# Kernel optimization log

Hardware: AMD Instinct MI355X
Metric: run time of the kernel (lower is better)

The kernel has to match this reference:

```python
import jax, jax.numpy as jnp
import numpy as np

TEMP = 10.0  # softmax_ called with N=10.0 in reduce_func

def qmul(a, b):
    # Hamilton product, rows are (w, x, y, z)
    aw, ax, ay, az = a[..., 0], a[..., 1], a[..., 2], a[..., 3]
    bw, bx, by, bz = b[..., 0], b[..., 1], b[..., 2], b[..., 3]
    return jnp.stack([
        aw * bw - ax * bx - ay * by - az * bz,
        aw * bx + ax * bw + ay * bz - az * by,
        aw * by - ax * bz + ay * bw + az * bx,
        aw * bz + ax * by - ay * bx + az * bw,
    ], axis=-1)

def setup_inputs() -> dict:
    key = jax.random.key(0)
    k1, k2, k3, k4, k5, k6 = jax.random.split(key, 6)
    N, E = 100000, 3200000
    node_levels = jax.random.uniform(k1, (N,), dtype=jnp.float32)
    node_q = jax.random.normal(k2, (N, 4), dtype=jnp.float32)
    node_q = node_q / jnp.linalg.norm(node_q, axis=1, keepdims=True)
    edge_rel_q = jax.random.normal(k3, (E, 4), dtype=jnp.float32)
    edge_rel_q = edge_rel_q / jnp.linalg.norm(edge_rel_q, axis=1, keepdims=True)
    edge_w = jax.random.uniform(k4, (E,), dtype=jnp.float32)
    src = jax.random.randint(k5, (E,), 0, N, dtype=jnp.int32)
    dst = jax.random.randint(k6, (E,), 0, N, dtype=jnp.int32)
    return {"node_levels": node_levels, "node_q": node_q,
            "edge_rel_q": edge_rel_q, "edge_w": edge_w,
            "src": src, "dst": dst}

def reference(node_levels, node_q, edge_rel_q, edge_w, src, dst):
    N = node_q.shape[0]
    # per-edge message: accumulated quaternion rel_q * q_src
    accu_q = qmul(edge_rel_q, node_q[src])          # [E,4]
    l_src = node_levels[src]                        # [E]
    # softmax logits: cost = w * l (self term has w = 1)
    cost_e = TEMP * edge_w * l_src                  # [E]
    cost_self = TEMP * node_levels                  # [N]
    # segmented stable softmax over {self} U in-edges per dst node
    seg_max = jax.ops.segment_max(cost_e, dst, num_segments=N)
    m = jnp.maximum(seg_max, cost_self)             # [N]
    exp_e = jnp.exp(cost_e - m[dst])                # [E]
    exp_self = jnp.exp(cost_self - m)               # [N]
    Z = jax.ops.segment_sum(exp_e, dst, num_segments=N) + exp_self
    # weighted sums
    sum_q = jax.ops.segment_sum(exp_e[:, None] * accu_q, dst, num_segments=N) \
            + exp_self[:, None] * node_q            # [N,4]
    sum_l = jax.ops.segment_sum(exp_e * l_src, dst, num_segments=N) \
            + exp_self * node_levels                # [N]
    out_q = sum_q / Z[:, None]
    out_levels = sum_l / Z
    # F.normalize(q, p=2, dim=1) with eps=1e-12 clamp
    norm = jnp.maximum(jnp.linalg.norm(out_q, axis=1, keepdims=True), 1e-12)
    return out_q / norm, out_levels
```

## Files before the change

### kernel.cpp

```cpp
#include <hip/hip_runtime.h>
#include <hip/hip_fp16.h>

#define TEMP 10.0f
#define TPB 512
#define HTPB 256
#define NBLK 768
#define SHIFT 9
#define GSZ 512
#define BMAX 256
#define TILE 2048
#define GTPB 1024
#define CAP 44

typedef float v2f  __attribute__((ext_vector_type(2)));
typedef float vf4  __attribute__((ext_vector_type(4)));
typedef unsigned uv4 __attribute__((ext_vector_type(4)));

__device__ __forceinline__ int   nt_i (const int* p)   { return __builtin_nontemporal_load(p); }
__device__ __forceinline__ float nt_f (const float* p) { return __builtin_nontemporal_load(p); }
__device__ __forceinline__ float4 nt_f4(const float4* p) {
    vf4 v = __builtin_nontemporal_load((const vf4*)p);
    return make_float4(v.x, v.y, v.z, v.w);
}
__device__ __forceinline__ uint4 nt_u4(const uint4* p) {
    uv4 v = __builtin_nontemporal_load((const uv4*)p);
    uint4 r; r.x = v.x; r.y = v.y; r.z = v.z; r.w = v.w; return r;
}

__device__ __forceinline__ void pk_fadd(float* p, float a, float b) {
#if __has_builtin(__builtin_amdgcn_global_atomic_fadd_v2f32)
    v2f v; v.x = a; v.y = b;
    __builtin_amdgcn_global_atomic_fadd_v2f32(
        (__attribute__((address_space(1))) v2f*)p, v);
#else
    atomicAdd(p, a); atomicAdd(p + 1, b);
#endif
}

__device__ __forceinline__ void hamilton(float4 a, float4 b,
                                         float& ow, float& ox, float& oy, float& oz) {
    ow = a.x*b.x - a.y*b.y - a.z*b.z - a.w*b.w;
    ox = a.x*b.y + a.y*b.x + a.z*b.w - a.w*b.z;
    oy = a.x*b.z - a.y*b.w + a.z*b.x + a.w*b.y;
    oz = a.x*b.w + a.y*b.z - a.z*b.y + a.w*b.x;
}

__device__ __forceinline__ unsigned f2h(float x) {
    return (unsigned)__half_as_ushort(__float2half_rn(x));
}
__device__ __forceinline__ float h2f(unsigned u) {
    return __half2float(__ushort_as_half((unsigned short)(u & 0xFFFFu)));
}

__global__ void __launch_bounds__(HTPB)
hist_kernel(const int* __restrict__ dst, unsigned* __restrict__ blkhist,
            int E, int B, int span) {
    extern __shared__ unsigned h[];
    for (int i = threadIdx.x; i < B; i += blockDim.x) h[i] = 0;
    __syncthreads();
    int start = blockIdx.x * span;
    int end = start + span; if (end > E) end = E;
    for (int e = start + threadIdx.x; e < end; e += blockDim.x)
        atomicAdd(&h[((unsigned)nt_i(&dst[e])) >> SHIFT], 1u);
    __syncthreads();
    for (int i = threadIdx.x; i < B; i += blockDim.x)
        blkhist[(size_t)i * gridDim.x + blockIdx.x] = h[i];
}

__global__ void __launch_bounds__(1024)
scan_blocks_kernel(unsigned* __restrict__ blkhist, unsigned* __restrict__ totals) {
    __shared__ unsigned s[1024];
    int b = blockIdx.x, t = threadIdx.x, n = blockDim.x;
    unsigned v = blkhist[(size_t)b * n + t];
    s[t] = v; __syncthreads();
    for (int off = 1; off < n; off <<= 1) {
        unsigned add = (t >= off) ? s[t - off] : 0u;
        __syncthreads();
        s[t] += add;
        __syncthreads();
    }
    blkhist[(size_t)b * n + t] = s[t] - v;
    if (t == n - 1) totals[b] = s[t];
}

__global__ void __launch_bounds__(1024)
scan_totals_kernel(const unsigned* __restrict__ totals,
                   unsigned* __restrict__ offsets, int B) {
    __shared__ unsigned s[1024];
    int t = threadIdx.x;
    unsigned v = (t < B) ? totals[t] : 0u;
    s[t] = v; __syncthreads();
    for (int off = 1; off < 1024; off <<= 1) {
        unsigned add = (t >= off) ? s[t - off] : 0u;
        __syncthreads();
        s[t] += add;
        __syncthreads();
    }
    if (t < B) offsets[t] = s[t] - v;
    if (t == B - 1) offsets[B] = s[t];
}

__global__ void __launch_bounds__(TPB)
scatter_sort_kernel(const float* __restrict__ nl, const float4* __restrict__ nq,
                    const float4* __restrict__ erq, const float* __restrict__ ew,
                    const int* __restrict__ src, const int* __restrict__ dst,
                    const unsigned* __restrict__ blkhist,
                    const unsigned* __restrict__ offsets,
                    uint4* __restrict__ buckets,
                    int E, int B, int span) {
    __shared__ uint4    stage[TILE];
    __shared__ unsigned gslot[TILE];
    __shared__ unsigned gcur[BMAX];
    __shared__ unsigned th[BMAX];
    __shared__ unsigned basec[BMAX];
    __shared__ unsigned curt[BMAX];

    int blk = blockIdx.x, nb = gridDim.x, tid = threadIdx.x;
    for (int b = tid; b < B; b += TPB)
        gcur[b] = offsets[b] + blkhist[(size_t)b * nb + blk];
    int start = blk * span;
    int end = start + span; if (end > E) end = E;

    for (int ts = start; ts < end; ts += TILE) {
        int tE = end - ts; if (tE > TILE) tE = TILE;
        for (int b = tid; b < B; b += TPB) th[b] = 0;
        __syncthreads();
        for (int k = tid; k < tE; k += TPB)
            atomicAdd(&th[((unsigned)dst[ts + k]) >> SHIFT], 1u);
        __syncthreads();
        if (tid < 64) {
            int lane = tid;
            unsigned vals[4];
            unsigned tot = 0;
            #pragma unroll
            for (int c = 0; c < 4; ++c) {
                int i = lane * 4 + c;
                vals[c] = (i < B) ? th[i] : 0u;
                tot += vals[c];
            }
            unsigned inc = tot;
            #pragma unroll
            for (int off = 1; off < 64; off <<= 1) {
                unsigned up = __shfl_up(inc, off);
                if (lane >= off) inc += up;
            }
            unsigned run = inc - tot;
            #pragma unroll
            for (int c = 0; c < 4; ++c) {
                int i = lane * 4 + c;
                if (i < B) { basec[i] = run; curt[i] = run; }
                run += vals[c];
            }
        }
        __syncthreads();
        for (int k = tid; k < tE; k += TPB) {
            int e = ts + k;
            int s_ = nt_i(&src[e]);
            unsigned d = (unsigned)dst[e];
            float l = nl[s_];
            float p = __expf(TEMP * nt_f(&ew[e]) * l);
            float ow, ox, oy, oz;
            hamilton(nt_f4(&erq[e]), nq[s_], ow, ox, oy, oz);
            unsigned b = d >> SHIFT;
            unsigned pos = atomicAdd(&curt[b], 1u);
            uint4 pk;
            pk.x = (d & (GSZ - 1)) | (f2h(p) << 16);
            pk.y = f2h(p * l)  | (f2h(p * ow) << 16);
            pk.z = f2h(p * ox) | (f2h(p * oy) << 16);
            pk.w = f2h(p * oz);
            stage[pos] = pk;
            gslot[pos] = gcur[b] + (pos - basec[b]);
        }
        __syncthreads();
        for (int k = tid; k < tE; k += TPB)
            buckets[gslot[k]] = stage[k];
        __syncthreads();
        for (int b = tid; b < B; b += TPB) gcur[b] += th[b];
        __syncthreads();
    }
}

__global__ void __launch_bounds__(GTPB)
gather_pay_kernel(const float* __restrict__ nl, const float4* __restrict__ nq,
                  const unsigned* __restrict__ offsets,
                  const uint4* __restrict__ buckets,
                  float4* __restrict__ out_q, float* __restrict__ out_l, int N) {
    __shared__ unsigned short idx[GSZ * CAP];
    __shared__ int   curn[GSZ];
    __shared__ float ovf[GSZ * 7];
    int b = blockIdx.x, tid = threadIdx.x;
    for (int i = tid; i < GSZ; i += GTPB) curn[i] = 0;
    for (int i = tid; i < GSZ * 7; i += GTPB) ovf[i] = 0.f;
    __syncthreads();

    unsigned s0 = offsets[b], s1 = offsets[b + 1];
    int M = (int)(s1 - s0);
    const unsigned* bx = (const unsigned*)(buckets + s0);

    for (int i = tid; i < M; i += GTPB) {
        unsigned w0 = bx[4 * (size_t)i];
        unsigned dl = w0 & (GSZ - 1);
        int slot = atomicAdd(&curn[dl], 1);
        if (slot < CAP) {
            idx[dl * CAP + slot] = (unsigned short)i;
        } else {
            uint4 pk = buckets[s0 + i];
            float* a = &ovf[dl * 7];
            atomicAdd(a + 0, h2f(pk.x >> 16));
            atomicAdd(a + 1, h2f(pk.y));
            atomicAdd(a + 2, h2f(pk.y >> 16));
            atomicAdd(a + 3, h2f(pk.z));
            atomicAdd(a + 4, h2f(pk.z >> 16));
            atomicAdd(a + 5, h2f(pk.w));
        }
    }
    __syncthreads();

    for (int half = 0; half < (GSZ * 4) / GTPB; ++half) {
        int j = half * (GTPB / 4) + (tid >> 2);
        int r = tid & 3;
        int deg = curn[j]; if (deg > CAP) deg = CAP;
        float aZ = 0.f, aL = 0.f, a0 = 0.f, a1 = 0.f, a2 = 0.f, a3 = 0.f;
        for (int s = r; s < deg; s += 4) {
            int i = idx[j * CAP + s];
            uint4 pk = nt_u4(&buckets[s0 + i]);
            aZ += h2f(pk.x >> 16);
            aL += h2f(pk.y);
            a0 += h2f(pk.y >> 16);
            a1 += h2f(pk.z);
            a2 += h2f(pk.z >> 16);
            a3 += h2f(pk.w);
        }
        for (int m = 1; m <= 2; m <<= 1) {
            aZ += __shfl_xor(aZ, m); aL += __shfl_xor(aL, m);
            a0 += __shfl_xor(a0, m); a1 += __shfl_xor(a1, m);
            a2 += __shfl_xor(a2, m); a3 += __shfl_xor(a3, m);
        }
        if (r == 0) {
            int n = b * GSZ + j;
            if (n < N) {
                const float* o = &ovf[j * 7];
                float l = nl[n];
                float ps = __expf(TEMP * l);
                float Z  = aZ + o[0] + ps;
                float sl = aL + o[1] + ps * l;
                float4 q = nq[n];
                float qw = a0 + o[2] + ps * q.x;
                float qx = a1 + o[3] + ps * q.y;
                float qy = a2 + o[4] + ps * q.z;
                float qz = a3 + o[5] + ps * q.w;
                float inv = 1.0f / Z;
                qw *= inv; qx *= inv; qy *= inv; qz *= inv;
                float norm = fmaxf(sqrtf(qw*qw + qx*qx + qy*qy + qz*qz), 1e-12f);
                float rn = 1.0f / norm;
                out_q[n] = make_float4(qw * rn, qx * rn, qy * rn, qz * rn);
                out_l[n] = sl * inv;
            }
        }
    }
}

__global__ void __launch_bounds__(256)
scatter_kernel(const int* __restrict__ dst, int* __restrict__ cnt,
               int* __restrict__ bucket, int cap,
               const float* __restrict__ node_levels, const float4* __restrict__ node_q,
               const float4* __restrict__ edge_rel_q, const float* __restrict__ edge_w,
               const int* __restrict__ src, float* __restrict__ side, int E) {
    int e = blockIdx.x * blockDim.x + threadIdx.x;
    if (e >= E) return;
    int d = dst[e];
    int slot = atomicAdd(&cnt[d], 1);
    if (slot < cap) {
        bucket[(long long)d * cap + slot] = e;
    } else {
        int s = src[e];
        float l = node_levels[s];
        float p = __expf(TEMP * edge_w[e] * l);
        float ow, ox, oy, oz;
        hamilton(edge_rel_q[e], node_q[s], ow, ox, oy, oz);
        float* rec = side + 6 * (long long)d;
        pk_fadd(rec + 0, p,      p * l);
        pk_fadd(rec + 2, p * ow, p * ox);
        pk_fadd(rec + 4, p * oy, p * oz);
    }
}

__global__ void __launch_bounds__(256)
gather_kernel(const float* __restrict__ node_levels, const float4* __restrict__ node_q,
              const float4* __restrict__ edge_rel_q, const float* __restrict__ edge_w,
              const int* __restrict__ src, const int* __restrict__ cnt,
              const int* __restrict__ bucket, int cap, const float* __restrict__ side,
              float4* __restrict__ out_q, float* __restrict__ out_l, int N) {
    int tid  = blockIdx.x * blockDim.x + threadIdx.x;
    int wave = tid >> 6, lane = tid & 63, half = lane >> 5, sub = lane & 31;
    int n = wave * 2 + half;
    float aZ = 0.f, aL = 0.f, a0 = 0.f, a1 = 0.f, a2 = 0.f, a3 = 0.f;
    if (n < N) {
        int deg = cnt[n]; if (deg > cap) deg = cap;
        const int* bkt = bucket + (long long)n * cap;
        for (int s = sub; s < deg; s += 32) {
            int e = bkt[s];
            int sn = src[e];
            float l = node_levels[sn];
            float p = __expf(TEMP * edge_w[e] * l);
            float ow, ox, oy, oz;
            hamilton(edge_rel_q[e], node_q[sn], ow, ox, oy, oz);
            aZ += p; aL += p * l; a0 += p * ow; a1 += p * ox; a2 += p * oy; a3 += p * oz;
        }
    }
    for (int m = 16; m; m >>= 1) {
        aZ += __shfl_xor(aZ, m); aL += __shfl_xor(aL, m);
        a0 += __shfl_xor(a0, m); a1 += __shfl_xor(a1, m);
        a2 += __shfl_xor(a2, m); a3 += __shfl_xor(a3, m);
    }
    if (sub == 0 && n < N) {
        const float* rec = side + 6 * (long long)n;
        float l  = node_levels[n];
        float ps = __expf(TEMP * l);
        float Z  = aZ + rec[0] + ps;
        float sl = aL + rec[1] + ps * l;
        float4 q = node_q[n];
        float qw = a0 + rec[2] + ps * q.x;
        float qx = a1 + rec[3] + ps * q.y;
        float qy = a2 + rec[4] + ps * q.z;
        float qz = a3 + rec[5] + ps * q.w;
        float inv = 1.0f / Z;
        qw *= inv; qx *= inv; qy *= inv; qz *= inv;
        float norm = fmaxf(sqrtf(qw*qw + qx*qx + qy*qy + qz*qz), 1e-12f);
        float rn = 1.0f / norm;
        out_q[n] = make_float4(qw * rn, qx * rn, qy * rn, qz * rn);
        out_l[n] = sl * inv;
    }
}

extern "C" void kernel_launch(void* const* d_in, const int* in_sizes, int n_in,
                              void* d_out, int out_size, void* d_ws, size_t ws_size,
                              hipStream_t stream) {
    const float*  node_levels = (const float*)d_in[0];
    const float4* node_q      = (const float4*)d_in[1];
    const float4* edge_rel_q  = (const float4*)d_in[2];
    const float*  edge_w      = (const float*)d_in[3];
    const int*    src         = (const int*)d_in[4];
    const int*    dst         = (const int*)d_in[5];

    const int N = in_sizes[0];
    const int E = in_sizes[3];

    const int B = (N + GSZ - 1) / GSZ;
    const int span = (E + NBLK - 1) / NBLK;

    size_t head_elems   = (size_t)B * NBLK + B + (B + 1);
    size_t buckets_byte = (head_elems * 4 + 15) & ~(size_t)15;
    size_t need         = buckets_byte + (size_t)E * 16;

    bool seg_ok = ((size_t)E / (size_t)B) < 32768;

    if (need <= ws_size && B <= BMAX && seg_ok) {
        unsigned* blkhist = (unsigned*)d_ws;
        unsigned* totals  = blkhist + (size_t)B * NBLK;
        unsigned* offsets = totals + B;
        uint4*    buckets = (uint4*)((char*)d_ws + buckets_byte);

        hist_kernel<<<NBLK, HTPB, B * 4, stream>>>(dst, blkhist, E, B, span);
        scan_blocks_kernel<<<B, NBLK, 0, stream>>>(blkhist, totals);
        scan_totals_kernel<<<1, 1024, 0, stream>>>(totals, offsets, B);
        scatter_sort_kernel<<<NBLK, TPB, 0, stream>>>(
            node_levels, node_q, edge_rel_q, edge_w, src, dst,
            blkhist, offsets, buckets, E, B, span);
        gather_pay_kernel<<<B, GTPB, 0, stream>>>(
            node_levels, node_q, offsets, buckets,
            (float4*)d_out, (float*)d_out + 4 * (long long)N, N);
    } else {
        const int tpb = 256;
        size_t cnt_elems  = ((size_t)N + 3) & ~(size_t)3;
        size_t side_elems = 6 * (size_t)N;
        size_t head_bytes = (cnt_elems + side_elems) * 4;
        int cap = 0;
        for (int c : {128, 64}) {
            if (head_bytes + (size_t)N * c * 4 <= ws_size) { cap = c; break; }
        }
        int*   cnt    = (int*)d_ws;
        float* side   = (float*)d_ws + cnt_elems;
        int*   bucket = (int*)d_ws + cnt_elems + side_elems;
        hipMemsetAsync(d_ws, 0, head_bytes, stream);
        scatter_kernel<<<(E + tpb - 1) / tpb, tpb, 0, stream>>>(
            dst, cnt, bucket, cap, node_levels, node_q, edge_rel_q, edge_w, src, side, E);
        int waves  = (N + 1) / 2;
        int blocks = (waves * 64 + tpb - 1) / tpb;
        gather_kernel<<<blocks, tpb, 0, stream>>>(
            node_levels, node_q, edge_rel_q, edge_w, src, cnt, bucket, cap, side,
            (float4*)d_out, (float*)d_out + 4 * (long long)N, N);
    }
}
```

Measured before the change: 236.7 us.

## Replace histogram-scan bucket sort with atomic slot reservation into fixed-capacity buckets

Drops the separate histogram and two scan kernels. The scatter kernel now reserves per-bucket ranges with global atomics into fixed-capacity buckets, and anything past capacity spills to an overflow FIFO. Buckets shrink to 200 nodes, giving 500 gather blocks, and the payload moves to a 12-byte struct-of-arrays plus a 2-byte local-dst array instead of 16-byte packed records. This removes three launches and a pass over dst in exchange for global atomic contention and a capacity heuristic. Every gather block also scans the whole overflow FIFO, and entries beyond its 8192 limit are silently dropped.

```diff
diff --git a/kernel.cpp b/kernel.cpp
--- a/kernel.cpp
+++ b/kernel.cpp
@@ -1,30 +1,24 @@
 #include <hip/hip_runtime.h>
 #include <hip/hip_fp16.h>
+#include <cmath>
 
 #define TEMP 10.0f
 #define TPB 512
-#define HTPB 256
-#define NBLK 768
-#define SHIFT 9
-#define GSZ 512
-#define BMAX 256
 #define TILE 2048
+#define GSZ 200
+#define BMAX 512
 #define GTPB 1024
 #define CAP 44
+#define OV 8192
 
 typedef float v2f  __attribute__((ext_vector_type(2)));
 typedef float vf4  __attribute__((ext_vector_type(4)));
-typedef unsigned uv4 __attribute__((ext_vector_type(4)));
 
 __device__ __forceinline__ int   nt_i (const int* p)   { return __builtin_nontemporal_load(p); }
 __device__ __forceinline__ float nt_f (const float* p) { return __builtin_nontemporal_load(p); }
 __device__ __forceinline__ float4 nt_f4(const float4* p) {
     vf4 v = __builtin_nontemporal_load((const vf4*)p);
     return make_float4(v.x, v.y, v.z, v.w);
-}
-__device__ __forceinline__ uint4 nt_u4(const uint4* p) {
-    uv4 v = __builtin_nontemporal_load((const uv4*)p);
-    uint4 r; r.x = v.x; r.y = v.y; r.z = v.z; r.w = v.w; return r;
 }
 
 __device__ __forceinline__ void pk_fadd(float* p, float a, float b) {
@@ -52,184 +46,143 @@
     return __half2float(__ushort_as_half((unsigned short)(u & 0xFFFFu)));
 }
 
-__global__ void __launch_bounds__(HTPB)
-hist_kernel(const int* __restrict__ dst, unsigned* __restrict__ blkhist,
-            int E, int B, int span) {
-    extern __shared__ unsigned h[];
-    for (int i = threadIdx.x; i < B; i += blockDim.x) h[i] = 0;
-    __syncthreads();
-    int start = blockIdx.x * span;
-    int end = start + span; if (end > E) end = E;
-    for (int e = start + threadIdx.x; e < end; e += blockDim.x)
-        atomicAdd(&h[((unsigned)nt_i(&dst[e])) >> SHIFT], 1u);
-    __syncthreads();
-    for (int i = threadIdx.x; i < B; i += blockDim.x)
-        blkhist[(size_t)i * gridDim.x + blockIdx.x] = h[i];
-}
-
-__global__ void __launch_bounds__(1024)
-scan_blocks_kernel(unsigned* __restrict__ blkhist, unsigned* __restrict__ totals) {
-    __shared__ unsigned s[1024];
-    int b = blockIdx.x, t = threadIdx.x, n = blockDim.x;
-    unsigned v = blkhist[(size_t)b * n + t];
-    s[t] = v; __syncthreads();
-    for (int off = 1; off < n; off <<= 1) {
-        unsigned add = (t >= off) ? s[t - off] : 0u;
-        __syncthreads();
-        s[t] += add;
-        __syncthreads();
-    }
-    blkhist[(size_t)b * n + t] = s[t] - v;
-    if (t == n - 1) totals[b] = s[t];
-}
-
-__global__ void __launch_bounds__(1024)
-scan_totals_kernel(const unsigned* __restrict__ totals,
-                   unsigned* __restrict__ offsets, int B) {
-    __shared__ unsigned s[1024];
-    int t = threadIdx.x;
-    unsigned v = (t < B) ? totals[t] : 0u;
-    s[t] = v; __syncthreads();
-    for (int off = 1; off < 1024; off <<= 1) {
-        unsigned add = (t >= off) ? s[t - off] : 0u;
-        __syncthreads();
-        s[t] += add;
-        __syncthreads();
-    }
-    if (t < B) offsets[t] = s[t] - v;
-    if (t == B - 1) offsets[B] = s[t];
-}
-
 __global__ void __launch_bounds__(TPB)
-scatter_sort_kernel(const float* __restrict__ nl, const float4* __restrict__ nq,
-                    const float4* __restrict__ erq, const float* __restrict__ ew,
-                    const int* __restrict__ src, const int* __restrict__ dst,
-                    const unsigned* __restrict__ blkhist,
-                    const unsigned* __restrict__ offsets,
-                    uint4* __restrict__ buckets,
-                    int E, int B, int span) {
-    __shared__ uint4    stage[TILE];
-    __shared__ unsigned gslot[TILE];
-    __shared__ unsigned gcur[BMAX];
-    __shared__ unsigned th[BMAX];
-    __shared__ unsigned basec[BMAX];
-    __shared__ unsigned curt[BMAX];
-
-    int blk = blockIdx.x, nb = gridDim.x, tid = threadIdx.x;
-    for (int b = tid; b < B; b += TPB)
-        gcur[b] = offsets[b] + blkhist[(size_t)b * nb + blk];
-    int start = blk * span;
-    int end = start + span; if (end > E) end = E;
-
-    for (int ts = start; ts < end; ts += TILE) {
-        int tE = end - ts; if (tE > TILE) tE = TILE;
-        for (int b = tid; b < B; b += TPB) th[b] = 0;
-        __syncthreads();
-        for (int k = tid; k < tE; k += TPB)
-            atomicAdd(&th[((unsigned)dst[ts + k]) >> SHIFT], 1u);
-        __syncthreads();
-        if (tid < 64) {
-            int lane = tid;
-            unsigned vals[4];
-            unsigned tot = 0;
-            #pragma unroll
-            for (int c = 0; c < 4; ++c) {
-                int i = lane * 4 + c;
-                vals[c] = (i < B) ? th[i] : 0u;
-                tot += vals[c];
+scatter_res_kernel(const float* __restrict__ nl, const float4* __restrict__ nq,
+                   const float4* __restrict__ erq, const float* __restrict__ ew,
+                   const int* __restrict__ src, const int* __restrict__ dst,
+                   unsigned* __restrict__ cnt, unsigned* __restrict__ ovfcur,
+                   uint4* __restrict__ fifo,
+                   unsigned* __restrict__ pay, unsigned short* __restrict__ dlarr,
+                   int E, int B, int capB) {
+    __shared__ unsigned sy[TILE], sz[TILE], sw[TILE], gsl[TILE];
+    __shared__ unsigned short sdl[TILE];
+    __shared__ unsigned th[BMAX], basec[BMAX], curt[BMAX], resv[BMAX];
+
+    int tid = threadIdx.x;
+    int ts = blockIdx.x * TILE;
+    int tE = E - ts; if (tE > TILE) tE = TILE;
+
+    for (int b = tid; b < B; b += TPB) th[b] = 0;
+    __syncthreads();
+    for (int k = tid; k < tE; k += TPB)
+        atomicAdd(&th[((unsigned)dst[ts + k]) / GSZ], 1u);
+    __syncthreads();
+    if (tid < 64) {
+        unsigned vals[8]; unsigned tot = 0;
+        #pragma unroll
+        for (int c = 0; c < 8; ++c) {
+            int i = tid * 8 + c;
+            vals[c] = (i < B) ? th[i] : 0u;
+            tot += vals[c];
+        }
+        unsigned inc = tot;
+        #pragma unroll
+        for (int off = 1; off < 64; off <<= 1) {
+            unsigned up = __shfl_up(inc, off);
+            if (tid >= off) inc += up;
+        }
+        unsigned run = inc - tot;
+        #pragma unroll
+        for (int c = 0; c < 8; ++c) {
+            int i = tid * 8 + c;
+            if (i < B) {
+                basec[i] = run; curt[i] = run;
+                resv[i] = vals[c] ? atomicAdd(&cnt[i], vals[c]) : 0u;
             }
-            unsigned inc = tot;
-            #pragma unroll
-            for (int off = 1; off < 64; off <<= 1) {
-                unsigned up = __shfl_up(inc, off);
-                if (lane >= off) inc += up;
-            }
-            unsigned run = inc - tot;
-            #pragma unroll
-            for (int c = 0; c < 4; ++c) {
-                int i = lane * 4 + c;
-                if (i < B) { basec[i] = run; curt[i] = run; }
-                run += vals[c];
-            }
-        }
-        __syncthreads();
-        for (int k = tid; k < tE; k += TPB) {
-            int e = ts + k;
-            int s_ = nt_i(&src[e]);
-            unsigned d = (unsigned)dst[e];
-            float l = nl[s_];
-            float p = __expf(TEMP * nt_f(&ew[e]) * l);
-            float ow, ox, oy, oz;
-            hamilton(nt_f4(&erq[e]), nq[s_], ow, ox, oy, oz);
-            unsigned b = d >> SHIFT;
-            unsigned pos = atomicAdd(&curt[b], 1u);
-            uint4 pk;
-            pk.x = (d & (GSZ - 1)) | (f2h(p) << 16);
-            pk.y = f2h(p * l)  | (f2h(p * ow) << 16);
-            pk.z = f2h(p * ox) | (f2h(p * oy) << 16);
-            pk.w = f2h(p * oz);
-            stage[pos] = pk;
-            gslot[pos] = gcur[b] + (pos - basec[b]);
-        }
-        __syncthreads();
-        for (int k = tid; k < tE; k += TPB)
-            buckets[gslot[k]] = stage[k];
-        __syncthreads();
-        for (int b = tid; b < B; b += TPB) gcur[b] += th[b];
-        __syncthreads();
+            run += vals[c];
+        }
+    }
+    __syncthreads();
+    for (int k = tid; k < tE; k += TPB) {
+        int e = ts + k;
+        int s_ = nt_i(&src[e]);
+        unsigned d = (unsigned)dst[e];
+        float l = nl[s_];
+        float p = __expf(TEMP * nt_f(&ew[e]) * l);
+        float ow, ox, oy, oz;
+        hamilton(nt_f4(&erq[e]), nq[s_], ow, ox, oy, oz);
+        unsigned bu = d / GSZ;
+        unsigned pos = atomicAdd(&curt[bu], 1u);
+        unsigned y = f2h(p)      | (f2h(p * l)  << 16);
+        unsigned z = f2h(p * ow) | (f2h(p * ox) << 16);
+        unsigned w = f2h(p * oy) | (f2h(p * oz) << 16);
+        sy[pos] = y; sz[pos] = z; sw[pos] = w;
+        sdl[pos] = (unsigned short)(d - bu * GSZ);
+        unsigned off = resv[bu] + (pos - basec[bu]);
+        if (off < (unsigned)capB) {
+            gsl[pos] = bu * (unsigned)capB + off;
+        } else {
+            gsl[pos] = 0xFFFFFFFFu;
+            unsigned o = atomicAdd(ovfcur, 1u);
+            if (o < OV) { uint4 f; f.x = d; f.y = y; f.z = z; f.w = w; fifo[o] = f; }
+        }
+    }
+    __syncthreads();
+    for (int k = tid; k < tE; k += TPB) {
+        unsigned g = gsl[k];
+        if (g != 0xFFFFFFFFu) {
+            size_t base = 3 * (size_t)g;
+            pay[base] = sy[k]; pay[base + 1] = sz[k]; pay[base + 2] = sw[k];
+            dlarr[g] = sdl[k];
+        }
     }
 }
 
 __global__ void __launch_bounds__(GTPB)
-gather_pay_kernel(const float* __restrict__ nl, const float4* __restrict__ nq,
-                  const unsigned* __restrict__ offsets,
-                  const uint4* __restrict__ buckets,
+gather_seg_kernel(const float* __restrict__ nl, const float4* __restrict__ nq,
+                  const unsigned* __restrict__ cnt, const unsigned* __restrict__ ovfcur,
+                  const uint4* __restrict__ fifo,
+                  const unsigned* __restrict__ pay, const unsigned short* __restrict__ dlarr,
+                  int capB,
                   float4* __restrict__ out_q, float* __restrict__ out_l, int N) {
     __shared__ unsigned short idx[GSZ * CAP];
     __shared__ int   curn[GSZ];
-    __shared__ float ovf[GSZ * 7];
+    __shared__ float ovfa[GSZ * 7];
     int b = blockIdx.x, tid = threadIdx.x;
     for (int i = tid; i < GSZ; i += GTPB) curn[i] = 0;
-    for (int i = tid; i < GSZ * 7; i += GTPB) ovf[i] = 0.f;
-    __syncthreads();
-
-    unsigned s0 = offsets[b], s1 = offsets[b + 1];
-    int M = (int)(s1 - s0);
-    const unsigned* bx = (const unsigned*)(buckets + s0);
+    for (int i = tid; i < GSZ * 7; i += GTPB) ovfa[i] = 0.f;
+    __syncthreads();
+
+    int M = (int)cnt[b]; if (M > capB) M = capB;
+    const unsigned* pb = pay + 3 * (size_t)b * capB;
+    const unsigned short* db = dlarr + (size_t)b * capB;
 
     for (int i = tid; i < M; i += GTPB) {
-        unsigned w0 = bx[4 * (size_t)i];
-        unsigned dl = w0 & (GSZ - 1);
+        int dl = db[i];
         int slot = atomicAdd(&curn[dl], 1);
         if (slot < CAP) {
             idx[dl * CAP + slot] = (unsigned short)i;
         } else {
-            uint4 pk = buckets[s0 + i];
-            float* a = &ovf[dl * 7];
-            atomicAdd(a + 0, h2f(pk.x >> 16));
-            atomicAdd(a + 1, h2f(pk.y));
-            atomicAdd(a + 2, h2f(pk.y >> 16));
-            atomicAdd(a + 3, h2f(pk.z));
-            atomicAdd(a + 4, h2f(pk.z >> 16));
-            atomicAdd(a + 5, h2f(pk.w));
-        }
-    }
-    __syncthreads();
-
-    for (int half = 0; half < (GSZ * 4) / GTPB; ++half) {
-        int j = half * (GTPB / 4) + (tid >> 2);
-        int r = tid & 3;
+            unsigned y = pb[3*(size_t)i], z = pb[3*(size_t)i+1], w = pb[3*(size_t)i+2];
+            float* a = &ovfa[dl * 7];
+            atomicAdd(a + 0, h2f(y)); atomicAdd(a + 1, h2f(y >> 16));
+            atomicAdd(a + 2, h2f(z)); atomicAdd(a + 3, h2f(z >> 16));
+            atomicAdd(a + 4, h2f(w)); atomicAdd(a + 5, h2f(w >> 16));
+        }
+    }
+    unsigned on = *ovfcur; if (on > OV) on = OV;
+    for (unsigned i = tid; i < on; i += GTPB) {
+        uint4 f = fifo[i];
+        unsigned loc = f.x - (unsigned)b * GSZ;
+        if (loc < GSZ) {
+            float* a = &ovfa[loc * 7];
+            atomicAdd(a + 0, h2f(f.y)); atomicAdd(a + 1, h2f(f.y >> 16));
+            atomicAdd(a + 2, h2f(f.z)); atomicAdd(a + 3, h2f(f.z >> 16));
+            atomicAdd(a + 4, h2f(f.w)); atomicAdd(a + 5, h2f(f.w >> 16));
+        }
+    }
+    __syncthreads();
+
+    int j = tid >> 2, r = tid & 3;
+    if (j < GSZ) {
         int deg = curn[j]; if (deg > CAP) deg = CAP;
         float aZ = 0.f, aL = 0.f, a0 = 0.f, a1 = 0.f, a2 = 0.f, a3 = 0.f;
         for (int s = r; s < deg; s += 4) {
             int i = idx[j * CAP + s];
-            uint4 pk = nt_u4(&buckets[s0 + i]);
-            aZ += h2f(pk.x >> 16);
-            aL += h2f(pk.y);
-            a0 += h2f(pk.y >> 16);
-            a1 += h2f(pk.z);
-            a2 += h2f(pk.z >> 16);
-            a3 += h2f(pk.w);
+            unsigned y = pb[3*(size_t)i], z = pb[3*(size_t)i+1], w = pb[3*(size_t)i+2];
+            aZ += h2f(y); aL += h2f(y >> 16);
+            a0 += h2f(z); a1 += h2f(z >> 16);
+            a2 += h2f(w); a3 += h2f(w >> 16);
         }
         for (int m = 1; m <= 2; m <<= 1) {
             aZ += __shfl_xor(aZ, m); aL += __shfl_xor(aL, m);
@@ -239,7 +192,7 @@
         if (r == 0) {
             int n = b * GSZ + j;
             if (n < N) {
-                const float* o = &ovf[j * 7];
+                const float* o = &ovfa[j * 7];
                 float l = nl[n];
                 float ps = __expf(TEMP * l);
                 float Z  = aZ + o[0] + ps;
@@ -347,28 +300,30 @@
     const int E = in_sizes[3];
 
     const int B = (N + GSZ - 1) / GSZ;
-    const int span = (E + NBLK - 1) / NBLK;
-
-    size_t head_elems   = (size_t)B * NBLK + B + (B + 1);
-    size_t buckets_byte = (head_elems * 4 + 15) & ~(size_t)15;
-    size_t need         = buckets_byte + (size_t)E * 16;
-
-    bool seg_ok = ((size_t)E / (size_t)B) < 32768;
-
-    if (need <= ws_size && B <= BMAX && seg_ok) {
-        unsigned* blkhist = (unsigned*)d_ws;
-        unsigned* totals  = blkhist + (size_t)B * NBLK;
-        unsigned* offsets = totals + B;
-        uint4*    buckets = (uint4*)((char*)d_ws + buckets_byte);
-
-        hist_kernel<<<NBLK, HTPB, B * 4, stream>>>(dst, blkhist, E, B, span);
-        scan_blocks_kernel<<<B, NBLK, 0, stream>>>(blkhist, totals);
-        scan_totals_kernel<<<1, 1024, 0, stream>>>(totals, offsets, B);
-        scatter_sort_kernel<<<NBLK, TPB, 0, stream>>>(
+
+    size_t fifo_off = (((size_t)(B + 1) * 4) + 15) & ~(size_t)15;
+    size_t pay_off  = fifo_off + (size_t)OV * 16;
+
+    long long availCap = ((long long)ws_size - (long long)pay_off) / (14LL * B);
+    int meanB  = E / B;
+    int minCap = meanB + 6 * (int)std::sqrt((double)meanB) + 8;
+    int capB   = (availCap > 16000) ? 16000 : (int)availCap;
+
+    if (capB >= minCap && B <= BMAX && meanB < 32000) {
+        unsigned*       cnt    = (unsigned*)d_ws;
+        unsigned*       ovfc   = cnt + B;
+        uint4*          fifo   = (uint4*)((char*)d_ws + fifo_off);
+        unsigned*       pay    = (unsigned*)((char*)d_ws + pay_off);
+        unsigned short* dlarr  = (unsigned short*)((char*)d_ws + pay_off + 12ull * B * capB);
+
+        hipMemsetAsync(d_ws, 0, (size_t)(B + 1) * 4, stream);
+
+        int nblk = (E + TILE - 1) / TILE;
+        scatter_res_kernel<<<nblk, TPB, 0, stream>>>(
             node_levels, node_q, edge_rel_q, edge_w, src, dst,
-            blkhist, offsets, buckets, E, B, span);
-        gather_pay_kernel<<<B, GTPB, 0, stream>>>(
-            node_levels, node_q, offsets, buckets,
+            cnt, ovfc, fifo, pay, dlarr, E, B, capB);
+        gather_seg_kernel<<<B, GTPB, 0, stream>>>(
+            node_levels, node_q, cnt, ovfc, fifo, pay, dlarr, capB,
             (float4*)d_out, (float*)d_out + 4 * (long long)N, N);
     } else {
         const int tpb = 256;
@@ -379,16 +334,16 @@
         for (int c : {128, 64}) {
             if (head_bytes + (size_t)N * c * 4 <= ws_size) { cap = c; break; }
         }
-        int*   cnt    = (int*)d_ws;
+        int*   fcnt   = (int*)d_ws;
         float* side   = (float*)d_ws + cnt_elems;
         int*   bucket = (int*)d_ws + cnt_elems + side_elems;
         hipMemsetAsync(d_ws, 0, head_bytes, stream);
         scatter_kernel<<<(E + tpb - 1) / tpb, tpb, 0, stream>>>(
-            dst, cnt, bucket, cap, node_levels, node_q, edge_rel_q, edge_w, src, side, E);
+            dst, fcnt, bucket, cap, node_levels, node_q, edge_rel_q, edge_w, src, side, E);
         int waves  = (N + 1) / 2;
         int blocks = (waves * 64 + tpb - 1) / tpb;
         gather_kernel<<<blocks, tpb, 0, stream>>>(
-            node_levels, node_q, edge_rel_q, edge_w, src, cnt, bucket, cap, side,
+            node_levels, node_q, edge_rel_q, edge_w, src, fcnt, bucket, cap, side,
             (float4*)d_out, (float*)d_out + 4 * (long long)N, N);
     }
 }
```

Measured after the change: 401.3 us. 69.5% more time.
